# Performance work log

Measured on AMD Instinct MI355X. Metric: run time of the kernel, lower is better.

The kernel has to match this reference:

```python
import jax, jax.numpy as jnp
import numpy as np

IN_C, OUT_C, NUM_VARS = 8, 8, 3
MODES1, MODES2 = 16, 16
TDIM = 256
B, H, W = 16, 256, 256
SCALE = 1.0 / (IN_C * OUT_C)


def setup_inputs() -> dict:
    key = jax.random.key(0)
    k1, k2, k3, k4, k5, k6 = jax.random.split(key, 6)
    wshape = (IN_C, OUT_C, NUM_VARS, MODES1, MODES2, TDIM)
    return {
        "t": jax.random.uniform(k1, (B, TDIM), dtype=jnp.float32),
        "x": jax.random.normal(k2, (B, IN_C, NUM_VARS, H, W), dtype=jnp.float32),
        "w1r": SCALE * jax.random.uniform(k3, wshape, dtype=jnp.float32),
        "w1i": SCALE * jax.random.uniform(k4, wshape, dtype=jnp.float32),
        "w2r": SCALE * jax.random.uniform(k5, wshape, dtype=jnp.float32),
        "w2i": SCALE * jax.random.uniform(k6, wshape, dtype=jnp.float32),
    }


def reference(t, x, w1r, w1i, w2r, w2i):
    m1, m2 = MODES1, MODES2
    b, _, v, h, w = x.shape
    wf = w // 2 + 1
    w1 = (w1r + 1j * w1i).astype(jnp.complex64)
    w2 = (w2r + 1j * w2i).astype(jnp.complex64)
    tc = t.astype(jnp.complex64)

    # FFT over last two spatial axes: [b, i, v, h, wf]
    x_ft = jnp.fft.rfft2(x)

    # time-conditioned spectral weights: [b, i, o, v, m1, m2]
    tw1 = jnp.einsum("bt,iovxyt->biovxy", tc, w1)
    tw2 = jnp.einsum("bt,iovxyt->biovxy", tc, w2)

    # complex spectral mixing on the retained low/high modes
    top = jnp.einsum("bivxy,biovxy->bovxy", x_ft[:, :, :, :m1, :m2], tw1)
    bot = jnp.einsum("bivxy,biovxy->bovxy", x_ft[:, :, :, -m1:, :m2], tw2)

    out_ft = jnp.zeros((b, OUT_C, v, h, wf), dtype=jnp.complex64)
    out_ft = out_ft.at[:, :, :, :m1, :m2].set(top)
    out_ft = out_ft.at[:, :, :, -m1:, :m2].set(bot)

    return jnp.fft.irfft2(out_ft, s=(h, w))
```

## Files before the change

kernel.cpp:

```cpp
#include <hip/hip_runtime.h>

#define BB 16
#define IC 8
#define OC 8
#define NV 3
#define M1 16
#define M2 16
#define HH 256
#define WW 256
#define NIMG_IN  (BB*IC*NV)
#define NIMG_OUT (BB*OC*NV)
#define NROWS    (IC*OC*NV*M1*M2)
#define TWO_PI 6.28318530717958647692f

__global__ __launch_bounds__(256, 4) void k1a_rowdft(const float* __restrict__ x,
                                                     float2* __restrict__ y) {
  __shared__ float2 tbl[256];
  __shared__ float red[2][64][73];
  const int tid = threadIdx.x;
  const int img = blockIdx.x >> 1;
  const int half = blockIdx.x & 1;
  const int kbase = half ? 9 : 0;
  const int kcount = half ? 8 : 9;
  {
    float s, c;
    sincosf((float)tid * (TWO_PI / 256.0f), &s, &c);
    tbl[tid] = make_float2(c, s);
  }
  __syncthreads();

  const int col4 = tid & 63;
  const int hq = tid >> 6;
  const float4* xp = (const float4*)(x + (size_t)img * 65536) + col4;

  float ar[9][4], ai[9][4];
#pragma unroll
  for (int j = 0; j < 9; j++)
#pragma unroll
    for (int c = 0; c < 4; c++) { ar[j][c] = 0.0f; ai[j][c] = 0.0f; }

  for (int hi = 0; hi < 64; hi++) {
    const int h = hq * 64 + hi;
    float4 xv = xp[(size_t)h * 64];
    int m = (kbase * h) & 255;
#pragma unroll
    for (int j = 0; j < 9; j++) {
      float2 e = tbl[m];
      m = (m + h) & 255;
      ar[j][0] = fmaf(e.x, xv.x, ar[j][0]);
      ai[j][0] = fmaf(-e.y, xv.x, ai[j][0]);
      ar[j][1] = fmaf(e.x, xv.y, ar[j][1]);
      ai[j][1] = fmaf(-e.y, xv.y, ai[j][1]);
      ar[j][2] = fmaf(e.x, xv.z, ar[j][2]);
      ai[j][2] = fmaf(-e.y, xv.z, ai[j][2]);
      ar[j][3] = fmaf(e.x, xv.w, ar[j][3]);
      ai[j][3] = fmaf(-e.y, xv.w, ai[j][3]);
    }
  }

  if (hq >= 2) {
    float* p = red[hq - 2][col4];
#pragma unroll
    for (int j = 0; j < 9; j++)
#pragma unroll
      for (int c = 0; c < 4; c++) { p[j * 8 + c * 2] = ar[j][c]; p[j * 8 + c * 2 + 1] = ai[j][c]; }
  }
  __syncthreads();
  if (hq < 2) {
    const float* p = red[hq][col4];
#pragma unroll
    for (int j = 0; j < 9; j++)
#pragma unroll
      for (int c = 0; c < 4; c++) { ar[j][c] += p[j * 8 + c * 2]; ai[j][c] += p[j * 8 + c * 2 + 1]; }
  }
  __syncthreads();
  if (hq == 1) {
    float* p = red[0][col4];
#pragma unroll
    for (int j = 0; j < 9; j++)
#pragma unroll
      for (int c = 0; c < 4; c++) { p[j * 8 + c * 2] = ar[j][c]; p[j * 8 + c * 2 + 1] = ai[j][c]; }
  }
  __syncthreads();
  if (hq == 0) {
    const float* p = red[0][col4];
    float2* yo = y + (size_t)img * 4352;
    for (int j = 0; j < kcount; j++) {
#pragma unroll
      for (int c = 0; c < 4; c++) {
        float rr = ar[j][c] + p[j * 8 + c * 2];
        float ii = ai[j][c] + p[j * 8 + c * 2 + 1];
        yo[(kbase + j) * 256 + col4 * 4 + c] = make_float2(rr, ii);
      }
    }
  }
}

__global__ __launch_bounds__(256) void k1b_coldft(const float2* __restrict__ y,
                                                  float2* __restrict__ Xf) {
  __shared__ float2 tbl[256];
  __shared__ float2 yb[17 * 257];
  const int tid = threadIdx.x;
  const int img = blockIdx.x;
  {
    float s, c;
    sincosf((float)tid * (TWO_PI / 256.0f), &s, &c);
    tbl[tid] = make_float2(c, s);
  }
  const float2* yg = y + (size_t)img * 4352;
  for (int n = tid; n < 4352; n += 256) {
    int kx = n >> 8, w = n & 255;
    yb[kx * 257 + w] = yg[n];
  }
  __syncthreads();

  float2* XfImg = Xf + (size_t)img * 512;
  for (int n = tid; n < 512; n += 256) {
    int row = n >> 4, ky = n & 15;
    int kxl = (row < 16) ? row : (32 - row);
    float sgn = (row < 16) ? 1.0f : -1.0f;
    float Xr = 0.0f, Xi = 0.0f;
    int m = 0;
    for (int w2 = 0; w2 < 256; w2++) {
      float2 yv = yb[kxl * 257 + w2];
      float2 e = tbl[m];
      m = (m + ky) & 255;
      float yy = yv.y * sgn;
      Xr += yv.x * e.x + yy * e.y;
      Xi += yy * e.x - yv.x * e.y;
    }
    XfImg[n] = make_float2(Xr, Xi);
  }
}

__global__ __launch_bounds__(256) void k2_tw(const float* __restrict__ t,
                                             const float* __restrict__ w1r,
                                             const float* __restrict__ w1i,
                                             const float* __restrict__ w2r,
                                             const float* __restrict__ w2i,
                                             float2* __restrict__ tw1,
                                             float2* __restrict__ tw2) {
  __shared__ float tL[16 * 260];
  __shared__ float4 wA[2][16 * 64];
  const int tid = threadIdx.x;
  const int row0 = blockIdx.x * 16;
  const int b = tid >> 4;
  const int r = tid & 15;
  const int c = r & 7;

  {
    const float4* tg = (const float4*)t;
    float4* ts = (float4*)tL;
    for (int n = tid; n < 1024; n += 256) ts[(n >> 6) * 65 + (n & 63)] = tg[n];
  }

  float o1r, o1i, o2r, o2i;
  const float4* tb4 = (const float4*)tL + b * 65;

  for (int pass = 0; pass < 2; pass++) {
    const float* wa = pass ? w2r : w1r;
    const float* wb = pass ? w2i : w1i;
    const float4* ga = (const float4*)(wa + (size_t)row0 * 256);
    const float4* gb = (const float4*)(wb + (size_t)row0 * 256);
    for (int n = tid; n < 1024; n += 256) {
      int rr = n >> 6, t4 = n & 63;
      int sidx = (rr << 6) | (t4 ^ (rr & 7));
      wA[0][sidx] = ga[n];
      wA[1][sidx] = gb[n];
    }
    __syncthreads();

    const float4* ra4 = wA[0] + (r << 6);
    const float4* rb4 = wA[1] + (r << 6);
    float arr = 0.0f, aii = 0.0f;
#pragma unroll 8
    for (int t4 = 0; t4 < 64; t4++) {
      float4 tv = tb4[t4];
      int s = t4 ^ c;
      float4 va = ra4[s];
      float4 vb = rb4[s];
      arr += tv.x * va.x + tv.y * va.y + tv.z * va.z + tv.w * va.w;
      aii += tv.x * vb.x + tv.y * vb.y + tv.z * vb.z + tv.w * vb.w;
    }
    if (pass) { o2r = arr; o2i = aii; } else { o1r = arr; o1i = aii; }
    __syncthreads();
  }

  tw1[(size_t)b * NROWS + row0 + r] = make_float2(o1r, o1i);
  tw2[(size_t)b * NROWS + row0 + r] = make_float2(o2r, o2i);
}

__global__ __launch_bounds__(256) void k3_mix(const float2* __restrict__ Xf,
                                              const float2* __restrict__ tw1,
                                              const float2* __restrict__ tw2,
                                              float2* __restrict__ ftT,
                                              float2* __restrict__ ftB) {
  const int n = blockIdx.x * 256 + threadIdx.x;
  const int xy = n & 255;
  const int ov = n >> 8;
  const int v = ov % 3;
  const int o = (ov / 3) & 7;
  const int b = n / (OC * NV * 256);

  float tr = 0.0f, ti2 = 0.0f, br = 0.0f, bi = 0.0f;
#pragma unroll
  for (int i = 0; i < IC; i++) {
    const float2 xt = Xf[(size_t)(((b * IC + i) * NV + v) << 9) + xy];
    const float2 xb = Xf[(size_t)(((b * IC + i) * NV + v) << 9) + 256 + xy];
    const int r = ((i * OC + o) * NV + v) * 256 + xy;
    float2 u1 = tw1[(size_t)b * NROWS + r];
    float2 u2 = tw2[(size_t)b * NROWS + r];
    tr += xt.x * u1.x - xt.y * u1.y;
    ti2 += xt.x * u1.y + xt.y * u1.x;
    br += xb.x * u2.x - xb.y * u2.y;
    bi += xb.x * u2.y + xb.y * u2.x;
  }
  const int nout = ((b * OC + o) * NV + v) * 256 + xy;
  ftT[nout] = make_float2(tr, ti2);
  ftB[nout] = make_float2(br, bi);
}

__global__ __launch_bounds__(256) void k4a_hdft(const float2* __restrict__ ftT,
                                                const float2* __restrict__ ftB,
                                                float2* __restrict__ G) {
  __shared__ float2 tbl[256];
  __shared__ float2 ftL[512];
  const int tid = threadIdx.x;
  const int img = blockIdx.x;
  {
    float s, c;
    sincosf((float)tid * (TWO_PI / 256.0f), &s, &c);
    tbl[tid] = make_float2(c, s);
    ftL[tid] = ftT[(size_t)img * 256 + tid];
    ftL[256 + tid] = ftB[(size_t)img * 256 + tid];
  }
  __syncthreads();

  const int h = tid;
  float gr[16], gi[16];
#pragma unroll
  for (int ky = 0; ky < 16; ky++) { gr[ky] = 0.0f; gi[ky] = 0.0f; }
  for (int row = 0; row < 32; row++) {
    int kxv = (row < 16) ? row : (224 + row);
    float2 e = tbl[(kxv * h) & 255];
#pragma unroll
    for (int ky = 0; ky < 16; ky++) {
      float2 f = ftL[row * 16 + ky];
      gr[ky] += f.x * e.x - f.y * e.y;
      gi[ky] += f.x * e.y + f.y * e.x;
    }
  }
  float2* Gi = G + (size_t)img * 4096;
#pragma unroll
  for (int ky = 0; ky < 16; ky++) Gi[ky * 256 + h] = make_float2(gr[ky], gi[ky]);
}

__global__ __launch_bounds__(256) void k4b_wdft(const float2* __restrict__ G,
                                                float* __restrict__ out) {
  __shared__ float2 tbl[256];
  __shared__ float2 PL[16 * 256];
  __shared__ float2 gt[512];
  const int tid = threadIdx.x;
  const int img = blockIdx.x >> 3;
  const int h0 = (blockIdx.x & 7) * 32;
  {
    float s, c;
    sincosf((float)tid * (TWO_PI / 256.0f), &s, &c);
    tbl[tid] = make_float2(c, s);
  }
  __syncthreads();
  for (int n = tid; n < 4096; n += 256) {
    int ky = n >> 8, w = n & 255;
    float2 e = tbl[(ky * w) & 255];
    float sc = (ky == 0) ? (1.0f / 65536.0f) : (2.0f / 65536.0f);
    PL[n] = make_float2(e.x * sc, e.y * sc);
  }
  const float2* Gi = G + (size_t)img * 4096;
  for (int n = tid; n < 512; n += 256) {
    int ky = n >> 5, hh = n & 31;
    gt[n] = Gi[ky * 256 + h0 + hh];
  }
  __syncthreads();

  const int w0 = tid & 63;
  const int hq = tid >> 6;
  float acc[8][4];
#pragma unroll
  for (int a = 0; a < 8; a++)
#pragma unroll
    for (int j = 0; j < 4; j++) acc[a][j] = 0.0f;

#pragma unroll 4
  for (int ky = 0; ky < 16; ky++) {
    float2 p0 = PL[ky * 256 + w0];
    float2 p1 = PL[ky * 256 + w0 + 64];
    float2 p2 = PL[ky * 256 + w0 + 128];
    float2 p3 = PL[ky * 256 + w0 + 192];
#pragma unroll
    for (int a = 0; a < 8; a++) {
      float2 g = gt[ky * 32 + hq * 8 + a];
      acc[a][0] += g.x * p0.x - g.y * p0.y;
      acc[a][1] += g.x * p1.x - g.y * p1.y;
      acc[a][2] += g.x * p2.x - g.y * p2.y;
      acc[a][3] += g.x * p3.x - g.y * p3.y;
    }
  }
  float* obase = out + (size_t)img * 65536 + (size_t)(h0 + hq * 8) * 256;
#pragma unroll
  for (int a = 0; a < 8; a++) {
#pragma unroll
    for (int j = 0; j < 4; j++) obase[a * 256 + w0 + 64 * j] = acc[a][j];
  }
}

extern "C" void kernel_launch(void* const* d_in, const int* in_sizes, int n_in,
                              void* d_out, int out_size, void* d_ws, size_t ws_size,
                              hipStream_t stream) {
  const float* t = (const float*)d_in[0];
  const float* x = (const float*)d_in[1];
  const float* w1r = (const float*)d_in[2];
  const float* w1i = (const float*)d_in[3];
  const float* w2r = (const float*)d_in[4];
  const float* w2i = (const float*)d_in[5];
  float* out = (float*)d_out;

  float2* R1 = (float2*)d_ws;
  float2* y = R1;
  float2* tw1 = R1;
  float2* tw2 = R1 + 786432;
  float2* G = R1;
  float2* Xf = R1 + 1671168;
  float2* ftT = Xf + 196608;
  float2* ftB = ftT + 98304;

  k1a_rowdft<<<NIMG_IN * 2, 256, 0, stream>>>(x, y);
  k1b_coldft<<<NIMG_IN, 256, 0, stream>>>(y, Xf);
  k2_tw<<<NROWS / 16, 256, 0, stream>>>(t, w1r, w1i, w2r, w2i, tw1, tw2);
  k3_mix<<<(BB * OC * NV * 256) / 256, 256, 0, stream>>>(Xf, tw1, tw2, ftT, ftB);
  k4a_hdft<<<NIMG_OUT, 256, 0, stream>>>(ftT, ftB, G);
  k4b_wdft<<<NIMG_OUT * 8, 256, 0, stream>>>(G, out);
}
```

Baseline: 469.0 us.

## Restructure row DFT kernel: 2 columns per thread, prefetch rows, simpler reduction

Result: faster. 426.8 us (-9.0%).

```diff
diff --git a/kernel.cpp b/kernel.cpp
--- a/kernel.cpp
+++ b/kernel.cpp
@@ -13,13 +13,38 @@
 #define NROWS    (IC*OC*NV*M1*M2)
 #define TWO_PI 6.28318530717958647692f
 
-__global__ __launch_bounds__(256, 4) void k1a_rowdft(const float* __restrict__ x,
+#define STEPJ(J, E, XV)                                   \
+  ar##J.x = fmaf((E).x, (XV).x, ar##J.x);                 \
+  ar##J.y = fmaf((E).x, (XV).y, ar##J.y);                 \
+  ai##J.x = fmaf(-(E).y, (XV).x, ai##J.x);                \
+  ai##J.y = fmaf(-(E).y, (XV).y, ai##J.y);
+
+#define ROW(XV, H) {                                      \
+  int m_ = (kbase * (H)) & 255;                           \
+  float2 e_;                                              \
+  e_ = tbl[m_]; STEPJ(0, e_, XV) m_ = (m_ + (H)) & 255;   \
+  e_ = tbl[m_]; STEPJ(1, e_, XV) m_ = (m_ + (H)) & 255;   \
+  e_ = tbl[m_]; STEPJ(2, e_, XV) m_ = (m_ + (H)) & 255;   \
+  e_ = tbl[m_]; STEPJ(3, e_, XV) m_ = (m_ + (H)) & 255;   \
+  e_ = tbl[m_]; STEPJ(4, e_, XV) m_ = (m_ + (H)) & 255;   \
+  e_ = tbl[m_]; STEPJ(5, e_, XV) m_ = (m_ + (H)) & 255;   \
+  e_ = tbl[m_]; STEPJ(6, e_, XV) m_ = (m_ + (H)) & 255;   \
+  e_ = tbl[m_]; STEPJ(7, e_, XV) m_ = (m_ + (H)) & 255;   \
+  e_ = tbl[m_]; STEPJ(8, e_, XV)                          \
+}
+
+#define STORJ(J) p[(J)*4+0]=ar##J.x; p[(J)*4+1]=ar##J.y; p[(J)*4+2]=ai##J.x; p[(J)*4+3]=ai##J.y;
+#define LOADJ(J) ar##J.x+=p[(J)*4+0]; ar##J.y+=p[(J)*4+1]; ai##J.x+=p[(J)*4+2]; ai##J.y+=p[(J)*4+3];
+#define OUTJ(J)  yo4[(kbase+(J))*128 + col2] = make_float4(ar##J.x, ai##J.x, ar##J.y, ai##J.y);
+
+__global__ __launch_bounds__(256, 3) void k1a_rowdft(const float* __restrict__ x,
                                                      float2* __restrict__ y) {
   __shared__ float2 tbl[256];
-  __shared__ float red[2][64][73];
-  const int tid = threadIdx.x;
-  const int img = blockIdx.x >> 1;
-  const int half = blockIdx.x & 1;
+  __shared__ float red[128][37];
+  const int tid = threadIdx.x;
+  const int bid = blockIdx.x;
+  const int half = (bid >= 384) ? 1 : 0;
+  const int img = bid - half * 384;
   const int kbase = half ? 9 : 0;
   const int kcount = half ? 8 : 9;
   {
@@ -29,70 +54,48 @@
   }
   __syncthreads();
 
-  const int col4 = tid & 63;
-  const int hq = tid >> 6;
-  const float4* xp = (const float4*)(x + (size_t)img * 65536) + col4;
-
-  float ar[9][4], ai[9][4];
-#pragma unroll
-  for (int j = 0; j < 9; j++)
-#pragma unroll
-    for (int c = 0; c < 4; c++) { ar[j][c] = 0.0f; ai[j][c] = 0.0f; }
-
-  for (int hi = 0; hi < 64; hi++) {
-    const int h = hq * 64 + hi;
-    float4 xv = xp[(size_t)h * 64];
-    int m = (kbase * h) & 255;
-#pragma unroll
-    for (int j = 0; j < 9; j++) {
-      float2 e = tbl[m];
-      m = (m + h) & 255;
-      ar[j][0] = fmaf(e.x, xv.x, ar[j][0]);
-      ai[j][0] = fmaf(-e.y, xv.x, ai[j][0]);
-      ar[j][1] = fmaf(e.x, xv.y, ar[j][1]);
-      ai[j][1] = fmaf(-e.y, xv.y, ai[j][1]);
-      ar[j][2] = fmaf(e.x, xv.z, ar[j][2]);
-      ai[j][2] = fmaf(-e.y, xv.z, ai[j][2]);
-      ar[j][3] = fmaf(e.x, xv.w, ar[j][3]);
-      ai[j][3] = fmaf(-e.y, xv.w, ai[j][3]);
-    }
-  }
-
-  if (hq >= 2) {
-    float* p = red[hq - 2][col4];
-#pragma unroll
-    for (int j = 0; j < 9; j++)
-#pragma unroll
-      for (int c = 0; c < 4; c++) { p[j * 8 + c * 2] = ar[j][c]; p[j * 8 + c * 2 + 1] = ai[j][c]; }
-  }
-  __syncthreads();
-  if (hq < 2) {
-    const float* p = red[hq][col4];
-#pragma unroll
-    for (int j = 0; j < 9; j++)
-#pragma unroll
-      for (int c = 0; c < 4; c++) { ar[j][c] += p[j * 8 + c * 2]; ai[j][c] += p[j * 8 + c * 2 + 1]; }
-  }
-  __syncthreads();
-  if (hq == 1) {
-    float* p = red[0][col4];
-#pragma unroll
-    for (int j = 0; j < 9; j++)
-#pragma unroll
-      for (int c = 0; c < 4; c++) { p[j * 8 + c * 2] = ar[j][c]; p[j * 8 + c * 2 + 1] = ai[j][c]; }
-  }
-  __syncthreads();
-  if (hq == 0) {
-    const float* p = red[0][col4];
-    float2* yo = y + (size_t)img * 4352;
-    for (int j = 0; j < kcount; j++) {
-#pragma unroll
-      for (int c = 0; c < 4; c++) {
-        float rr = ar[j][c] + p[j * 8 + c * 2];
-        float ii = ai[j][c] + p[j * 8 + c * 2 + 1];
-        yo[(kbase + j) * 256 + col4 * 4 + c] = make_float2(rr, ii);
-      }
-    }
+  const int col2 = tid & 127;
+  const int hq = tid >> 7;
+  const int hbase = hq * 128;
+  const float2* xp = (const float2*)(x + (size_t)img * 65536) + col2;
+
+  float2 ar0 = {0,0}, ar1 = {0,0}, ar2 = {0,0}, ar3 = {0,0}, ar4 = {0,0},
+         ar5 = {0,0}, ar6 = {0,0}, ar7 = {0,0}, ar8 = {0,0};
+  float2 ai0 = {0,0}, ai1 = {0,0}, ai2 = {0,0}, ai3 = {0,0}, ai4 = {0,0},
+         ai5 = {0,0}, ai6 = {0,0}, ai7 = {0,0}, ai8 = {0,0};
+
+  float2 c0 = xp[(size_t)(hbase + 0) * 128];
+  float2 c1 = xp[(size_t)(hbase + 1) * 128];
+  float2 c2 = xp[(size_t)(hbase + 2) * 128];
+  float2 c3 = xp[(size_t)(hbase + 3) * 128];
+
+  for (int hi = 0; hi < 128; hi += 4) {
+    const int hn = (hbase + hi + 4) & 255;
+    float2 n0 = xp[(size_t)(hn + 0) * 128];
+    float2 n1 = xp[(size_t)(hn + 1) * 128];
+    float2 n2 = xp[(size_t)(hn + 2) * 128];
+    float2 n3 = xp[(size_t)(hn + 3) * 128];
+
+    const int h = hbase + hi;
+    ROW(c0, h + 0)
+    ROW(c1, h + 1)
+    ROW(c2, h + 2)
+    ROW(c3, h + 3)
+
+    c0 = n0; c1 = n1; c2 = n2; c3 = n3;
+  }
+
+  if (hq) {
+    float* p = &red[col2][0];
+    STORJ(0) STORJ(1) STORJ(2) STORJ(3) STORJ(4) STORJ(5) STORJ(6) STORJ(7) STORJ(8)
+  }
+  __syncthreads();
+  if (!hq) {
+    const float* p = &red[col2][0];
+    LOADJ(0) LOADJ(1) LOADJ(2) LOADJ(3) LOADJ(4) LOADJ(5) LOADJ(6) LOADJ(7) LOADJ(8)
+    float4* yo4 = (float4*)(y + (size_t)img * 4352);
+    OUTJ(0) OUTJ(1) OUTJ(2) OUTJ(3) OUTJ(4) OUTJ(5) OUTJ(6) OUTJ(7)
+    if (kcount == 9) { OUTJ(8) }
   }
 }
 
```
